# Kernel optimization log

Hardware: AMD Instinct MI355X
Metric: run time of the kernel (lower is better)

## Reference

```python
import jax, jax.numpy as jnp
import numpy as np
import math

LATENT = 64
COMP = 20
EM_ITERS = 5
GAMMA1 = 1.0  # 1/sqrt(gamma), gamma=1
LOG_NORM_C = -0.5 * math.log(2.0 * math.pi)


def setup_inputs() -> dict:
    key = jax.random.key(0)
    k1, k2, k3 = jax.random.split(key, 3)
    z = jax.random.normal(k1, (64, 8192, LATENT), dtype=jnp.float32)
    # small causal adjacency so (I - A) and the inverses are well conditioned
    A = jax.random.normal(k2, (LATENT, LATENT), dtype=jnp.float32) * 0.05
    init_idx = jax.random.randint(k3, (64, COMP), 0, 8192)
    return {"z": z, "A": A, "init_idx": init_idx}


def _em_step(X, pi, mean, trace, IA):
    # X: [B,N,L], pi/trace: [B,K], mean: [B,K,L], IA = I - A: [L,L]
    B, N, L = X.shape
    # gaussian_log_prob(X, mean) with logvar=0, summed over L, expanded as
    # -0.5*||x-m||^2 + L*c, computed without materializing a [B,N,K,L] tensor
    sq_x = jnp.sum(X * X, axis=-1)                      # [B,N]
    sq_m = jnp.sum(mean * mean, axis=-1)                # [B,K]
    cross = jnp.einsum('bnl,bkl->bnk', X, mean)         # [B,N,K]
    term_x = -0.5 * (sq_x[:, :, None] - 2.0 * cross + sq_m[:, None, :]) + L * LOG_NORM_C
    # gaussian_log_prob(causal(mean), 0, logvar=log(trace) broadcast over L)
    cm = jnp.einsum('bkl,lm->bkm', mean, IA)            # causal(mean)
    lt = jnp.log(trace)                                  # [B,K]
    term_c = -0.5 * (L * lt + jnp.sum(cm * cm, axis=-1) / trace) + L * LOG_NORM_C
    ll = term_x + jnp.log(pi)[:, None, :] + term_c[:, None, :]   # [B,N,K]
    post = jax.nn.softmax(ll, axis=-1)
    Nk = jnp.sum(post, axis=1)                           # [B,K]
    Nk = jnp.where(Nk == 0.0, jnp.asarray(1e-22, Nk.dtype), Nk)
    new_trace = GAMMA1 * jnp.ones_like(Nk)
    # std_causal = causal(I*trace) = trace*(I-A); trace is gamma1 for every
    # (b,k), so the [B,K,L,L] inverse collapses to one shared [L,L] inverse.
    I = jnp.eye(L, dtype=X.dtype)
    M = jnp.linalg.inv(I + (GAMMA1 ** 2) * (IA @ IA.T))
    new_pi = Nk / jnp.sum(Nk, axis=-1, keepdims=True)    # fix_pi=False
    new_mean = jnp.einsum('bnk,bnl->bkl', post, X) / Nk[:, :, None]
    new_mean = jnp.einsum('bkl,lm->bkm', new_mean, M)
    return new_pi, new_mean, new_trace


def reference(z, A, init_idx):
    # EM-based Gaussian-mixture prior (get_unsupervised_prior) of GMVAE
    B, N, L = z.shape
    I = jnp.eye(L, dtype=z.dtype)
    IA = I - A  # linear CausalEncoder: causal(x) = x @ (I - A)
    pi = jnp.full((B, COMP), 1.0 / COMP, dtype=z.dtype)
    trace = jnp.ones((B, COMP), dtype=z.dtype)
    # initial inverse: inv(I + (1/trace) * sig_cas @ sig_cas.T), trace == 1
    M0 = jnp.linalg.inv(I + IA @ IA.T)
    mean = jnp.take_along_axis(z, init_idx[:, :, None], axis=1)  # [B,K,L]
    mean = jnp.einsum('bkl,lm->bkm', mean, M0)
    for _ in range(EM_ITERS):
        pi, mean, trace = _em_step(z, pi, mean, trace, IA)
    return pi, mean, trace
```

## Files before the change

### kernel.cpp

```cpp
#include <hip/hip_runtime.h>
#include <math.h>

#define BB 64
#define NN 8192
#define LL 64
#define KK 20
#define TILE 128
#define NT 8
#define CHUNKS 8
#define ZSB 72
#define ZTS 140
#define PTTS 136
#define AS 132
#define TS 68

typedef float f32x4 __attribute__((ext_vector_type(4)));
typedef short s16x8 __attribute__((ext_vector_type(8)));
typedef short s16x4 __attribute__((ext_vector_type(4)));
typedef unsigned short u16x4 __attribute__((ext_vector_type(4)));
typedef unsigned short u16x2 __attribute__((ext_vector_type(2)));

#define MFMA_BF16 __builtin_amdgcn_mfma_f32_16x16x32_bf16

__device__ __forceinline__ unsigned short f2bf(float f) {
    unsigned int u = __float_as_uint(f);
    u += 0x7fffu + ((u >> 16) & 1u);
    return (unsigned short)(u >> 16);
}
__device__ __forceinline__ float bf2f(unsigned short h) {
    return __uint_as_float(((unsigned int)h) << 16);
}


__global__ __launch_bounds__(256) void k_setup(const float* __restrict__ A,
                                               float* __restrict__ IA,
                                               float* __restrict__ M) {
    __shared__ __align__(16) float iaT[64][TS];
    __shared__ __align__(16) float aug[64][AS];
    __shared__ __align__(16) float prowbuf[2][AS];
    int t = threadIdx.x;
    for (int i = t; i < 4096; i += 256) {
        int r = i >> 6, c = i & 63;
        float v = (r == c ? 1.0f : 0.0f) - A[i];
        IA[i] = v;
        iaT[c][r] = v;
    }
    __syncthreads();
    {
        int r0 = (t >> 4) << 2;
        int c0 = (t & 15) << 2;
        float s[4][4];
        #pragma unroll
        for (int a = 0; a < 4; ++a)
            #pragma unroll
            for (int bq = 0; bq < 4; ++bq) s[a][bq] = 0.f;
        for (int l = 0; l < 64; ++l) {
            float4 u = *(const float4*)&iaT[l][r0];
            float4 v = *(const float4*)&iaT[l][c0];
            float uu[4] = {u.x, u.y, u.z, u.w};
            float vv[4] = {v.x, v.y, v.z, v.w};
            #pragma unroll
            for (int a = 0; a < 4; ++a)
                #pragma unroll
                for (int bq = 0; bq < 4; ++bq) s[a][bq] += uu[a] * vv[bq];
        }
        #pragma unroll
        for (int a = 0; a < 4; ++a) {
            int r = r0 + a;
            float4 w;
            w.x = s[a][0] + (r == c0 + 0 ? 1.f : 0.f);
            w.y = s[a][1] + (r == c0 + 1 ? 1.f : 0.f);
            w.z = s[a][2] + (r == c0 + 2 ? 1.f : 0.f);
            w.w = s[a][3] + (r == c0 + 3 ? 1.f : 0.f);
            *(float4*)&aug[r][c0] = w;
            float4 id;
            id.x = (r == c0 + 0 ? 1.f : 0.f);
            id.y = (r == c0 + 1 ? 1.f : 0.f);
            id.z = (r == c0 + 2 ? 1.f : 0.f);
            id.w = (r == c0 + 3 ? 1.f : 0.f);
            *(float4*)&aug[r][64 + c0] = id;
        }
    }
    __syncthreads();
    int r = t >> 2;
    int cbase = (t & 3) * 32;
    if (r == 0) {
        float pivinv = 1.0f / aug[0][0];
        #pragma unroll
        for (int i = 0; i < 8; ++i) {
            float4 v = *(const float4*)&aug[0][cbase + 4 * i];
            v.x *= pivinv; v.y *= pivinv; v.z *= pivinv; v.w *= pivinv;
            *(float4*)&prowbuf[0][cbase + 4 * i] = v;
        }
    }
    __syncthreads();
    for (int k = 0; k < 64; ++k) {
        const float* prow = prowbuf[k & 1];
        float* prown = prowbuf[(k + 1) & 1];
        if (r == k) {
            #pragma unroll
            for (int i = 0; i < 8; ++i)
                *(float4*)&aug[r][cbase + 4 * i] = *(const float4*)&prow[cbase + 4 * i];
        } else {
            float f = aug[r][k];
            float4 v[8];
            #pragma unroll
            for (int i = 0; i < 8; ++i) {
                float4 p = *(const float4*)&prow[cbase + 4 * i];
                float4 a = *(const float4*)&aug[r][cbase + 4 * i];
                a.x -= f * p.x; a.y -= f * p.y; a.z -= f * p.z; a.w -= f * p.w;
                *(float4*)&aug[r][cbase + 4 * i] = a;
                v[i] = a;
            }
            if (r == k + 1) {
                float pivinv = 1.0f / aug[k + 1][k + 1];
                #pragma unroll
                for (int i = 0; i < 8; ++i) {
                    float4 w = v[i];
                    w.x *= pivinv; w.y *= pivinv; w.z *= pivinv; w.w *= pivinv;
                    *(float4*)&prown[cbase + 4 * i] = w;
                }
            }
        }
        __syncthreads();
    }
    for (int i = t; i < 4096; i += 256) {
        int rr = i >> 6, c = i & 63;
        M[i] = aug[rr][64 + c];
    }
}

__global__ __launch_bounds__(64) void k_init(const float* __restrict__ z,
                                             const int* __restrict__ idxs,
                                             const float* __restrict__ M,
                                             const float* __restrict__ IA,
                                             float* __restrict__ out_mean,
                                             float* __restrict__ bias,
                                             float* __restrict__ nk,
                                             float* __restrict__ macc,
                                             int* __restrict__ cnt) {
    int k = blockIdx.x, b = blockIdx.y;
    int l = threadIdx.x;
    int bk = b * KK + k;
    __shared__ float srow[64];
    __shared__ float smean[64];
    int idx = idxs[bk];
    srow[l] = z[((size_t)b * NN + idx) * LL + l];
    __syncthreads();
    float nm = 0.f;
    #pragma unroll 8
    for (int m = 0; m < 64; ++m) nm += srow[m] * M[m * 64 + l];
    out_mean[(size_t)bk * LL + l] = nm;
    smean[l] = nm;
    __syncthreads();
    float cm = 0.f;
    #pragma unroll 8
    for (int m = 0; m < 64; ++m) cm += smean[m] * IA[m * 64 + l];
    float sqm = nm * nm;
    float sqc = cm * cm;
    for (int off = 32; off > 0; off >>= 1) {
        sqm += __shfl_down(sqm, off);
        sqc += __shfl_down(sqc, off);
    }
    if (l == 0) {
        bias[bk] = logf(1.0f / KK) - 0.5f * (sqm + sqc);
        nk[bk] = 0.f;
        if (k == 0) cnt[b] = 0;
    }
    macc[(size_t)bk * LL + l] = 0.f;
}

__global__ __launch_bounds__(256, 2) void k_empass(const float* __restrict__ z,
                                                   float* __restrict__ mean,
                                                   float* __restrict__ bias,
                                                   float* __restrict__ nk,
                                                   float* __restrict__ macc,
                                                   int* __restrict__ cnt,
                                                   const float* __restrict__ M,
                                                   const float* __restrict__ IA,
                                                   float* __restrict__ out_pi,
                                                   float* __restrict__ out_trace) {
    __shared__ __align__(16) unsigned short zhl[2][TILE][ZSB];
    __shared__ __align__(16) unsigned short mhl[2][32][ZSB];
    __shared__ __align__(16) unsigned short zT[64][ZTS];
    __shared__ __align__(16) unsigned short ptT[32][PTTS];
    __shared__ __align__(16) float bias_s[32];
    __shared__ float nkred[4][KK];
    __shared__ int isLast;
    int t = threadIdx.x;
    int lane = t & 63;
    int q = t >> 6;
    int ln = lane & 15;
    int lg4 = lane >> 4;
    int s = t & 15;
    int b = blockIdx.y;
    size_t zbase = ((size_t)b * NN + (size_t)blockIdx.x * (TILE * NT)) * LL;

    for (int i = t; i < KK * LL; i += 256) {
        float f = mean[(size_t)b * KK * LL + i];
        int k = i >> 6, c = i & 63;
        unsigned short h = f2bf(f);
        mhl[0][k][c] = h;
        mhl[1][k][c] = f2bf(f - bf2f(h));
    }
    for (int i = 20 * ZSB + t; i < 32 * ZSB; i += 256) {
        (&mhl[0][0][0])[i] = 0;
        (&mhl[1][0][0])[i] = 0;
    }
    {
        unsigned int* pz = (unsigned int*)&ptT[20][0];
        for (int i = t; i < 6 * PTTS; i += 256) pz[i] = 0;
    }
    if (t < 32) bias_s[t] = (t < KK) ? bias[b * KK + t] : -1e30f;
    __syncthreads();
    float4 b0 = *(const float4*)&bias_s[lg4 * 4];
    float4 b1 = *(const float4*)&bias_s[16 + lg4 * 4];

    const float4* zg = (const float4*)(z + zbase);
    f32x4 bacc0 = {0.f, 0.f, 0.f, 0.f};
    f32x4 bacc1 = {0.f, 0.f, 0.f, 0.f};
    float nkp0[4] = {0.f, 0.f, 0.f, 0.f};
    float nkp1[4] = {0.f, 0.f, 0.f, 0.f};

    for (int tt = 0; tt < NT; ++tt) {
        if (tt > 0) __syncthreads();
        #pragma unroll
        for (int u = 0; u < 4; ++u) {
            int r0 = u * 32 + ((t >> 4) << 1);
            float4 v0 = zg[tt * 2048 + r0 * 16 + s];
            float4 v1 = zg[tt * 2048 + (r0 + 1) * 16 + s];
            unsigned short h0 = f2bf(v0.x), h1 = f2bf(v0.y), h2 = f2bf(v0.z), h3 = f2bf(v0.w);
            unsigned short g0 = f2bf(v1.x), g1 = f2bf(v1.y), g2 = f2bf(v1.z), g3 = f2bf(v1.w);
            *(u16x4*)&zhl[0][r0][4 * s]     = (u16x4){h0, h1, h2, h3};
            *(u16x4*)&zhl[0][r0 + 1][4 * s] = (u16x4){g0, g1, g2, g3};
            *(u16x4*)&zhl[1][r0][4 * s]     = (u16x4){f2bf(v0.x - bf2f(h0)), f2bf(v0.y - bf2f(h1)),
                                                      f2bf(v0.z - bf2f(h2)), f2bf(v0.w - bf2f(h3))};
            *(u16x4*)&zhl[1][r0 + 1][4 * s] = (u16x4){f2bf(v1.x - bf2f(g0)), f2bf(v1.y - bf2f(g1)),
                                                      f2bf(v1.z - bf2f(g2)), f2bf(v1.w - bf2f(g3))};
            *(u16x2*)&zT[4 * s + 0][r0] = (u16x2){h0, g0};
            *(u16x2*)&zT[4 * s + 1][r0] = (u16x2){h1, g1};
            *(u16x2*)&zT[4 * s + 2][r0] = (u16x2){h2, g2};
            *(u16x2*)&zT[4 * s + 3][r0] = (u16x2){h3, g3};
        }
        __syncthreads();

        f32x4 acc0[2], acc1[2];
        #pragma unroll
        for (int rt = 0; rt < 2; ++rt) {
            acc0[rt] = (f32x4){b0.x, b0.y, b0.z, b0.w};
            acc1[rt] = (f32x4){b1.x, b1.y, b1.z, b1.w};
        }
        #pragma unroll
        for (int ks = 0; ks < 2; ++ks) {
            int kc = ks * 32 + lg4 * 8;
            s16x8 mh0 = *(const s16x8*)&mhl[0][ln][kc];
            s16x8 ml0 = *(const s16x8*)&mhl[1][ln][kc];
            s16x8 mh1 = *(const s16x8*)&mhl[0][16 + ln][kc];
            s16x8 ml1 = *(const s16x8*)&mhl[1][16 + ln][kc];
            #pragma unroll
            for (int rt = 0; rt < 2; ++rt) {
                int zrow = q * 32 + rt * 16 + ln;
                s16x8 zh = *(const s16x8*)&zhl[0][zrow][kc];
                s16x8 zl = *(const s16x8*)&zhl[1][zrow][kc];
                acc0[rt] = MFMA_BF16(mh0, zh, acc0[rt], 0, 0, 0);
                acc0[rt] = MFMA_BF16(ml0, zh, acc0[rt], 0, 0, 0);
                acc0[rt] = MFMA_BF16(mh0, zl, acc0[rt], 0, 0, 0);
                acc1[rt] = MFMA_BF16(mh1, zh, acc1[rt], 0, 0, 0);
                acc1[rt] = MFMA_BF16(ml1, zh, acc1[rt], 0, 0, 0);
                acc1[rt] = MFMA_BF16(mh1, zl, acc1[rt], 0, 0, 0);
            }
        }
        #pragma unroll
        for (int rt = 0; rt < 2; ++rt) {
            int zrow = q * 32 + rt * 16 + ln;
            float m = fmaxf(fmaxf(fmaxf(acc0[rt][0], acc0[rt][1]), fmaxf(acc0[rt][2], acc0[rt][3])),
                            fmaxf(fmaxf(acc1[rt][0], acc1[rt][1]), fmaxf(acc1[rt][2], acc1[rt][3])));
            m = fmaxf(m, __shfl_xor(m, 16));
            m = fmaxf(m, __shfl_xor(m, 32));
            float e0[4], e1[4];
            float sm = 0.f;
            #pragma unroll
            for (int j = 0; j < 4; ++j) {
                e0[j] = __expf(acc0[rt][j] - m); sm += e0[j];
                e1[j] = __expf(acc1[rt][j] - m); sm += e1[j];
            }
            sm += __shfl_xor(sm, 16);
            sm += __shfl_xor(sm, 32);
            float inv = 1.0f / sm;
            #pragma unroll
            for (int j = 0; j < 4; ++j) {
                float p = e0[j] * inv;
                nkp0[j] += p;
                ptT[lg4 * 4 + j][zrow] = f2bf(p);
            }
            if (lg4 == 0) {
                #pragma unroll
                for (int j = 0; j < 4; ++j) {
                    float p = e1[j] * inv;
                    nkp1[j] += p;
                    ptT[16 + j][zrow] = f2bf(p);
                }
            }
        }
        __syncthreads();

        #pragma unroll
        for (int ch = 0; ch < 4; ++ch) {
            int rr = ch * 32 + lg4 * 8;
            s16x4 zb0 = *(const s16x4*)&zT[q * 16 + ln][rr];
            s16x4 zb1 = *(const s16x4*)&zT[q * 16 + ln][rr + 4];
            s16x8 bfr = (s16x8){zb0[0], zb0[1], zb0[2], zb0[3], zb1[0], zb1[1], zb1[2], zb1[3]};
            s16x8 af0 = *(const s16x8*)&ptT[ln][rr];
            s16x8 af1 = *(const s16x8*)&ptT[16 + ln][rr];
            bacc0 = MFMA_BF16(af0, bfr, bacc0, 0, 0, 0);
            bacc1 = MFMA_BF16(af1, bfr, bacc1, 0, 0, 0);
        }
    }

    #pragma unroll
    for (int j = 0; j < 4; ++j) {
        nkp0[j] += __shfl_xor(nkp0[j], 1);
        nkp0[j] += __shfl_xor(nkp0[j], 2);
        nkp0[j] += __shfl_xor(nkp0[j], 4);
        nkp0[j] += __shfl_xor(nkp0[j], 8);
    }
    if (ln == 0) {
        #pragma unroll
        for (int j = 0; j < 4; ++j) nkred[q][lg4 * 4 + j] = nkp0[j];
    }
    if (lg4 == 0) {
        #pragma unroll
        for (int j = 0; j < 4; ++j) {
            nkp1[j] += __shfl_xor(nkp1[j], 1);
            nkp1[j] += __shfl_xor(nkp1[j], 2);
            nkp1[j] += __shfl_xor(nkp1[j], 4);
            nkp1[j] += __shfl_xor(nkp1[j], 8);
        }
        if (ln == 0) {
            #pragma unroll
            for (int j = 0; j < 4; ++j) nkred[q][16 + j] = nkp1[j];
        }
    }

    int col = q * 16 + ln;
    #pragma unroll
    for (int reg = 0; reg < 4; ++reg) {
        int comp = lg4 * 4 + reg;
        atomicAdd(&macc[((size_t)b * KK + comp) * LL + col], bacc0[reg]);
    }
    if (lg4 == 0) {
        #pragma unroll
        for (int reg = 0; reg < 4; ++reg)
            atomicAdd(&macc[((size_t)b * KK + 16 + reg) * LL + col], bacc1[reg]);
    }
    __syncthreads();
    if (t < KK) {
        float sum = nkred[0][t] + nkred[1][t] + nkred[2][t] + nkred[3][t];
        atomicAdd(&nk[b * KK + t], sum);
    }
    __syncthreads();
    if (t == 0) {
        __threadfence();
        int old = atomicAdd(&cnt[b], 1);
        isLast = (old == CHUNKS - 1) ? 1 : 0;
    }
    __syncthreads();
    if (!isLast) return;

    float* fs = (float*)&zhl[0][0][0];
    float* sraw = fs + q * 160;
    float* smean = sraw + 64;
    int l = lane;
    #pragma unroll
    for (int kc5 = 0; kc5 < 5; ++kc5) {
        int comp = kc5 * 4 + q;
        int bk = b * KK + comp;
        size_t mb = (size_t)bk * LL;
        float nkv = 0.f;
        if (l == 0) nkv = atomicExch(&nk[bk], 0.f);
        nkv = __shfl(nkv, 0);
        float nkc = fmaxf(nkv, 1e-22f);
        float raw = atomicExch(&macc[mb + l], 0.f) / nkc;
        sraw[l] = raw;
        float nm = 0.f;
        #pragma unroll 8
        for (int m = 0; m < 64; ++m) nm += sraw[m] * M[m * 64 + l];
        mean[mb + l] = nm;
        smean[l] = nm;
        float cm = 0.f;
        #pragma unroll 8
        for (int m = 0; m < 64; ++m) cm += smean[m] * IA[m * 64 + l];
        float sqm = nm * nm;
        float sqc = cm * cm;
        #pragma unroll
        for (int off = 32; off > 0; off >>= 1) {
            sqm += __shfl_down(sqm, off);
            sqc += __shfl_down(sqc, off);
        }
        if (l == 0) {
            float pi = nkc * (1.0f / NN);
            bias[bk] = logf(pi) - 0.5f * (sqm + sqc);
            out_pi[bk] = pi;
            out_trace[bk] = 1.0f;
        }
    }
    if (t == 0) cnt[b] = 0;
}

extern "C" void kernel_launch(void* const* d_in, const int* in_sizes, int n_in,
                              void* d_out, int out_size, void* d_ws, size_t ws_size,
                              hipStream_t stream) {
    const float* z = (const float*)d_in[0];
    const float* A = (const float*)d_in[1];
    const int* idxs = (const int*)d_in[2];

    float* out_pi = (float*)d_out;
    float* out_mean = out_pi + BB * KK;
    float* out_trace = out_mean + (size_t)BB * KK * LL;

    float* ws = (float*)d_ws;
    float* IA = ws;
    float* M = ws + 4096;
    float* bias = ws + 8192;
    float* nk = ws + 9472;
    float* macc = ws + 10752;
    int* cnt = (int*)(ws + 92672);

    k_setup<<<1, 256, 0, stream>>>(A, IA, M);
    k_init<<<dim3(KK, BB), 64, 0, stream>>>(z, idxs, M, IA, out_mean, bias, nk, macc, cnt);
    for (int it = 0; it < 5; ++it) {
        k_empass<<<dim3(CHUNKS, BB), 256, 0, stream>>>(z, out_mean, bias, nk, macc,
                                                       cnt, M, IA, out_pi, out_trace);
    }
}
```

Measured before the change: 377.3 us.

## Prefetch z tiles into registers, hoist mean fragments, use Newton-Schulz inverse

The main EM kernel now loads the next z tile into registers while it computes on the current one, then writes that tile to shared memory after the MFMA stage, with one fewer barrier per tile. The mean bf16 fragments are hoisted into registers outside the tile loop. The softmax write path is made branch-free, and the zero-fill of the padded rows of the posterior tile is removed. The setup kernel replaces serial Gauss-Jordan elimination with 8 Newton-Schulz iterations made of 64x64 matmuls. This shortens the setup critical path but adds an approximation risk if convergence is incomplete, and the mainloop keeps more values live in registers.

```diff
diff --git a/kernel.cpp b/kernel.cpp
--- a/kernel.cpp
+++ b/kernel.cpp
@@ -11,8 +11,7 @@
 #define ZSB 72
 #define ZTS 140
 #define PTTS 136
-#define AS 132
-#define TS 68
+#define NSS 68
 
 typedef float f32x4 __attribute__((ext_vector_type(4)));
 typedef short s16x8 __attribute__((ext_vector_type(8)));
@@ -35,34 +34,39 @@
 __global__ __launch_bounds__(256) void k_setup(const float* __restrict__ A,
                                                float* __restrict__ IA,
                                                float* __restrict__ M) {
-    __shared__ __align__(16) float iaT[64][TS];
-    __shared__ __align__(16) float aug[64][AS];
-    __shared__ __align__(16) float prowbuf[2][AS];
+    __shared__ __align__(16) float sS[64][NSS];
+    __shared__ __align__(16) float sXa[64][NSS];
+    __shared__ __align__(16) float sXb[64][NSS];
+    __shared__ __align__(16) float sT[64][NSS];
+    __shared__ float rowsum[64];
+    __shared__ float alpha_s;
     int t = threadIdx.x;
+    int r0 = (t >> 4) << 2;
+    int c0 = (t & 15) << 2;
+
     for (int i = t; i < 4096; i += 256) {
         int r = i >> 6, c = i & 63;
         float v = (r == c ? 1.0f : 0.0f) - A[i];
         IA[i] = v;
-        iaT[c][r] = v;
+        sT[c][r] = v;
     }
     __syncthreads();
     {
-        int r0 = (t >> 4) << 2;
-        int c0 = (t & 15) << 2;
         float s[4][4];
         #pragma unroll
         for (int a = 0; a < 4; ++a)
             #pragma unroll
-            for (int bq = 0; bq < 4; ++bq) s[a][bq] = 0.f;
+            for (int b = 0; b < 4; ++b) s[a][b] = 0.f;
+        #pragma unroll 4
         for (int l = 0; l < 64; ++l) {
-            float4 u = *(const float4*)&iaT[l][r0];
-            float4 v = *(const float4*)&iaT[l][c0];
+            float4 u = *(const float4*)&sT[l][r0];
+            float4 v = *(const float4*)&sT[l][c0];
             float uu[4] = {u.x, u.y, u.z, u.w};
             float vv[4] = {v.x, v.y, v.z, v.w};
             #pragma unroll
             for (int a = 0; a < 4; ++a)
                 #pragma unroll
-                for (int bq = 0; bq < 4; ++bq) s[a][bq] += uu[a] * vv[bq];
+                for (int b = 0; b < 4; ++b) s[a][b] += uu[a] * vv[b];
         }
         #pragma unroll
         for (int a = 0; a < 4; ++a) {
@@ -72,62 +76,91 @@
             w.y = s[a][1] + (r == c0 + 1 ? 1.f : 0.f);
             w.z = s[a][2] + (r == c0 + 2 ? 1.f : 0.f);
             w.w = s[a][3] + (r == c0 + 3 ? 1.f : 0.f);
-            *(float4*)&aug[r][c0] = w;
-            float4 id;
-            id.x = (r == c0 + 0 ? 1.f : 0.f);
-            id.y = (r == c0 + 1 ? 1.f : 0.f);
-            id.z = (r == c0 + 2 ? 1.f : 0.f);
-            id.w = (r == c0 + 3 ? 1.f : 0.f);
-            *(float4*)&aug[r][64 + c0] = id;
-        }
-    }
-    __syncthreads();
-    int r = t >> 2;
-    int cbase = (t & 3) * 32;
-    if (r == 0) {
-        float pivinv = 1.0f / aug[0][0];
-        #pragma unroll
-        for (int i = 0; i < 8; ++i) {
-            float4 v = *(const float4*)&aug[0][cbase + 4 * i];
-            v.x *= pivinv; v.y *= pivinv; v.z *= pivinv; v.w *= pivinv;
-            *(float4*)&prowbuf[0][cbase + 4 * i] = v;
-        }
-    }
-    __syncthreads();
-    for (int k = 0; k < 64; ++k) {
-        const float* prow = prowbuf[k & 1];
-        float* prown = prowbuf[(k + 1) & 1];
-        if (r == k) {
-            #pragma unroll
-            for (int i = 0; i < 8; ++i)
-                *(float4*)&aug[r][cbase + 4 * i] = *(const float4*)&prow[cbase + 4 * i];
-        } else {
-            float f = aug[r][k];
-            float4 v[8];
-            #pragma unroll
-            for (int i = 0; i < 8; ++i) {
-                float4 p = *(const float4*)&prow[cbase + 4 * i];
-                float4 a = *(const float4*)&aug[r][cbase + 4 * i];
-                a.x -= f * p.x; a.y -= f * p.y; a.z -= f * p.z; a.w -= f * p.w;
-                *(float4*)&aug[r][cbase + 4 * i] = a;
-                v[i] = a;
-            }
-            if (r == k + 1) {
-                float pivinv = 1.0f / aug[k + 1][k + 1];
+            *(float4*)&sS[r][c0] = w;
+        }
+    }
+    __syncthreads();
+    if (t < 64) {
+        float sm = 0.f;
+        #pragma unroll 4
+        for (int c = 0; c < 64; c += 4) {
+            float4 v = *(const float4*)&sS[t][c];
+            sm += fabsf(v.x) + fabsf(v.y) + fabsf(v.z) + fabsf(v.w);
+        }
+        rowsum[t] = sm;
+    }
+    __syncthreads();
+    if (t == 0) {
+        float mx = rowsum[0];
+        for (int i = 1; i < 64; ++i) mx = fmaxf(mx, rowsum[i]);
+        alpha_s = 2.0f / (1.0f + mx);
+    }
+    __syncthreads();
+    float alpha = alpha_s;
+    for (int i = t; i < 4096; i += 256) {
+        int r = i >> 6, c = i & 63;
+        sXa[r][c] = (r == c) ? alpha : 0.f;
+    }
+    __syncthreads();
+
+    float* X  = &sXa[0][0];
+    float* Xn = &sXb[0][0];
+    for (int it = 0; it < 8; ++it) {
+        {
+            float s[4][4];
+            #pragma unroll
+            for (int a = 0; a < 4; ++a)
                 #pragma unroll
-                for (int i = 0; i < 8; ++i) {
-                    float4 w = v[i];
-                    w.x *= pivinv; w.y *= pivinv; w.z *= pivinv; w.w *= pivinv;
-                    *(float4*)&prown[cbase + 4 * i] = w;
-                }
-            }
+                for (int b = 0; b < 4; ++b) s[a][b] = 0.f;
+            #pragma unroll 4
+            for (int k = 0; k < 64; ++k) {
+                float4 u = *(const float4*)&sS[k][r0];
+                float4 v = *(const float4*)&X[k * NSS + c0];
+                float uu[4] = {u.x, u.y, u.z, u.w};
+                float vv[4] = {v.x, v.y, v.z, v.w};
+                #pragma unroll
+                for (int a = 0; a < 4; ++a)
+                    #pragma unroll
+                    for (int b = 0; b < 4; ++b) s[a][b] += uu[a] * vv[b];
+            }
+            #pragma unroll
+            for (int a = 0; a < 4; ++a)
+                *(float4*)&sT[r0 + a][c0] = (float4){s[a][0], s[a][1], s[a][2], s[a][3]};
         }
         __syncthreads();
-    }
-    for (int i = t; i < 4096; i += 256) {
-        int rr = i >> 6, c = i & 63;
-        M[i] = aug[rr][64 + c];
-    }
+        {
+            float s[4][4];
+            #pragma unroll
+            for (int a = 0; a < 4; ++a)
+                #pragma unroll
+                for (int b = 0; b < 4; ++b) s[a][b] = 0.f;
+            #pragma unroll 4
+            for (int k = 0; k < 64; ++k) {
+                float4 u = *(const float4*)&X[k * NSS + r0];
+                float4 v = *(const float4*)&sT[k][c0];
+                float uu[4] = {u.x, u.y, u.z, u.w};
+                float vv[4] = {v.x, v.y, v.z, v.w};
+                #pragma unroll
+                for (int a = 0; a < 4; ++a)
+                    #pragma unroll
+                    for (int b = 0; b < 4; ++b) s[a][b] += uu[a] * vv[b];
+            }
+            #pragma unroll
+            for (int a = 0; a < 4; ++a) {
+                float4 xo = *(const float4*)&X[(r0 + a) * NSS + c0];
+                float4 w;
+                w.x = 2.f * xo.x - s[a][0];
+                w.y = 2.f * xo.y - s[a][1];
+                w.z = 2.f * xo.z - s[a][2];
+                w.w = 2.f * xo.w - s[a][3];
+                *(float4*)&Xn[(r0 + a) * NSS + c0] = w;
+            }
+        }
+        __syncthreads();
+        float* tmp = X; X = Xn; Xn = tmp;
+    }
+    for (int i = t; i < 4096; i += 256)
+        M[i] = X[(i >> 6) * NSS + (i & 63)];
 }
 
 __global__ __launch_bounds__(64) void k_init(const float* __restrict__ z,
@@ -192,9 +225,9 @@
     int q = t >> 6;
     int ln = lane & 15;
     int lg4 = lane >> 4;
-    int s = t & 15;
     int b = blockIdx.y;
     size_t zbase = ((size_t)b * NN + (size_t)blockIdx.x * (TILE * NT)) * LL;
+    int rbase = 32 * q + 8 * lg4;
 
     for (int i = t; i < KK * LL; i += 256) {
         float f = mean[(size_t)b * KK * LL + i];
@@ -207,42 +240,77 @@
         (&mhl[0][0][0])[i] = 0;
         (&mhl[1][0][0])[i] = 0;
     }
-    {
-        unsigned int* pz = (unsigned int*)&ptT[20][0];
-        for (int i = t; i < 6 * PTTS; i += 256) pz[i] = 0;
-    }
     if (t < 32) bias_s[t] = (t < KK) ? bias[b * KK + t] : -1e30f;
     __syncthreads();
     float4 b0 = *(const float4*)&bias_s[lg4 * 4];
     float4 b1 = *(const float4*)&bias_s[16 + lg4 * 4];
+    s16x8 mf[8];
+    #pragma unroll
+    for (int ks = 0; ks < 2; ++ks) {
+        int kc = ks * 32 + lg4 * 8;
+        mf[ks * 4 + 0] = *(const s16x8*)&mhl[0][ln][kc];
+        mf[ks * 4 + 1] = *(const s16x8*)&mhl[1][ln][kc];
+        mf[ks * 4 + 2] = *(const s16x8*)&mhl[0][16 + ln][kc];
+        mf[ks * 4 + 3] = *(const s16x8*)&mhl[1][16 + ln][kc];
+    }
 
     const float4* zg = (const float4*)(z + zbase);
+    float4 pf[8];
+
+#define LOADT(tt)                                                              \
+    {                                                                          \
+        _Pragma("unroll")                                                      \
+        for (int u = 0; u < 4; ++u) {                                          \
+            int r0_ = rbase + 2 * u;                                           \
+            pf[2 * u]     = zg[(size_t)(tt) * 2048 + r0_ * 16 + ln];           \
+            pf[2 * u + 1] = zg[(size_t)(tt) * 2048 + (r0_ + 1) * 16 + ln];     \
+        }                                                                      \
+    }
+#define WRITE_ZHL                                                              \
+    {                                                                          \
+        _Pragma("unroll")                                                      \
+        for (int u = 0; u < 4; ++u) {                                          \
+            int r0_ = rbase + 2 * u;                                           \
+            float4 v0 = pf[2 * u], v1 = pf[2 * u + 1];                         \
+            unsigned short h0 = f2bf(v0.x), h1 = f2bf(v0.y),                   \
+                           h2 = f2bf(v0.z), h3 = f2bf(v0.w);                   \
+            unsigned short g0 = f2bf(v1.x), g1 = f2bf(v1.y),                   \
+                           g2 = f2bf(v1.z), g3 = f2bf(v1.w);                   \
+            *(u16x4*)&zhl[0][r0_][4 * ln]     = (u16x4){h0, h1, h2, h3};       \
+            *(u16x4*)&zhl[0][r0_ + 1][4 * ln] = (u16x4){g0, g1, g2, g3};       \
+            *(u16x4*)&zhl[1][r0_][4 * ln] =                                    \
+                (u16x4){f2bf(v0.x - bf2f(h0)), f2bf(v0.y - bf2f(h1)),          \
+                        f2bf(v0.z - bf2f(h2)), f2bf(v0.w - bf2f(h3))};         \
+            *(u16x4*)&zhl[1][r0_ + 1][4 * ln] =                                \
+                (u16x4){f2bf(v1.x - bf2f(g0)), f2bf(v1.y - bf2f(g1)),          \
+                        f2bf(v1.z - bf2f(g2)), f2bf(v1.w - bf2f(g3))};         \
+        }                                                                      \
+    }
+#define WRITE_ZT                                                               \
+    {                                                                          \
+        _Pragma("unroll")                                                      \
+        for (int u = 0; u < 4; ++u) {                                          \
+            int r0_ = rbase + 2 * u;                                           \
+            float4 v0 = pf[2 * u], v1 = pf[2 * u + 1];                         \
+            *(u16x2*)&zT[4 * ln + 0][r0_] = (u16x2){f2bf(v0.x), f2bf(v1.x)};   \
+            *(u16x2*)&zT[4 * ln + 1][r0_] = (u16x2){f2bf(v0.y), f2bf(v1.y)};   \
+            *(u16x2*)&zT[4 * ln + 2][r0_] = (u16x2){f2bf(v0.z), f2bf(v1.z)};   \
+            *(u16x2*)&zT[4 * ln + 3][r0_] = (u16x2){f2bf(v0.w), f2bf(v1.w)};   \
+        }                                                                      \
+    }
+
+    LOADT(0);
+    WRITE_ZHL;
+    WRITE_ZT;
+    __syncthreads();
+
     f32x4 bacc0 = {0.f, 0.f, 0.f, 0.f};
     f32x4 bacc1 = {0.f, 0.f, 0.f, 0.f};
     float nkp0[4] = {0.f, 0.f, 0.f, 0.f};
     float nkp1[4] = {0.f, 0.f, 0.f, 0.f};
 
     for (int tt = 0; tt < NT; ++tt) {
-        if (tt > 0) __syncthreads();
-        #pragma unroll
-        for (int u = 0; u < 4; ++u) {
-            int r0 = u * 32 + ((t >> 4) << 1);
-            float4 v0 = zg[tt * 2048 + r0 * 16 + s];
-            float4 v1 = zg[tt * 2048 + (r0 + 1) * 16 + s];
-            unsigned short h0 = f2bf(v0.x), h1 = f2bf(v0.y), h2 = f2bf(v0.z), h3 = f2bf(v0.w);
-            unsigned short g0 = f2bf(v1.x), g1 = f2bf(v1.y), g2 = f2bf(v1.z), g3 = f2bf(v1.w);
-            *(u16x4*)&zhl[0][r0][4 * s]     = (u16x4){h0, h1, h2, h3};
-            *(u16x4*)&zhl[0][r0 + 1][4 * s] = (u16x4){g0, g1, g2, g3};
-            *(u16x4*)&zhl[1][r0][4 * s]     = (u16x4){f2bf(v0.x - bf2f(h0)), f2bf(v0.y - bf2f(h1)),
-                                                      f2bf(v0.z - bf2f(h2)), f2bf(v0.w - bf2f(h3))};
-            *(u16x4*)&zhl[1][r0 + 1][4 * s] = (u16x4){f2bf(v1.x - bf2f(g0)), f2bf(v1.y - bf2f(g1)),
-                                                      f2bf(v1.z - bf2f(g2)), f2bf(v1.w - bf2f(g3))};
-            *(u16x2*)&zT[4 * s + 0][r0] = (u16x2){h0, g0};
-            *(u16x2*)&zT[4 * s + 1][r0] = (u16x2){h1, g1};
-            *(u16x2*)&zT[4 * s + 2][r0] = (u16x2){h2, g2};
-            *(u16x2*)&zT[4 * s + 3][r0] = (u16x2){h3, g3};
-        }
-        __syncthreads();
+        if (tt + 1 < NT) LOADT(tt + 1);
 
         f32x4 acc0[2], acc1[2];
         #pragma unroll
@@ -253,21 +321,17 @@
         #pragma unroll
         for (int ks = 0; ks < 2; ++ks) {
             int kc = ks * 32 + lg4 * 8;
-            s16x8 mh0 = *(const s16x8*)&mhl[0][ln][kc];
-            s16x8 ml0 = *(const s16x8*)&mhl[1][ln][kc];
-            s16x8 mh1 = *(const s16x8*)&mhl[0][16 + ln][kc];
-            s16x8 ml1 = *(const s16x8*)&mhl[1][16 + ln][kc];
             #pragma unroll
             for (int rt = 0; rt < 2; ++rt) {
                 int zrow = q * 32 + rt * 16 + ln;
                 s16x8 zh = *(const s16x8*)&zhl[0][zrow][kc];
                 s16x8 zl = *(const s16x8*)&zhl[1][zrow][kc];
-                acc0[rt] = MFMA_BF16(mh0, zh, acc0[rt], 0, 0, 0);
-                acc0[rt] = MFMA_BF16(ml0, zh, acc0[rt], 0, 0, 0);
-                acc0[rt] = MFMA_BF16(mh0, zl, acc0[rt], 0, 0, 0);
-                acc1[rt] = MFMA_BF16(mh1, zh, acc1[rt], 0, 0, 0);
-                acc1[rt] = MFMA_BF16(ml1, zh, acc1[rt], 0, 0, 0);
-                acc1[rt] = MFMA_BF16(mh1, zl, acc1[rt], 0, 0, 0);
+                acc0[rt] = MFMA_BF16(mf[ks * 4 + 0], zh, acc0[rt], 0, 0, 0);
+                acc0[rt] = MFMA_BF16(mf[ks * 4 + 1], zh, acc0[rt], 0, 0, 0);
+                acc0[rt] = MFMA_BF16(mf[ks * 4 + 0], zl, acc0[rt], 0, 0, 0);
+                acc1[rt] = MFMA_BF16(mf[ks * 4 + 2], zh, acc1[rt], 0, 0, 0);
+                acc1[rt] = MFMA_BF16(mf[ks * 4 + 3], zh, acc1[rt], 0, 0, 0);
+                acc1[rt] = MFMA_BF16(mf[ks * 4 + 2], zl, acc1[rt], 0, 0, 0);
             }
         }
         #pragma unroll
@@ -289,17 +353,12 @@
             float inv = 1.0f / sm;
             #pragma unroll
             for (int j = 0; j < 4; ++j) {
-                float p = e0[j] * inv;
-                nkp0[j] += p;
-                ptT[lg4 * 4 + j][zrow] = f2bf(p);
-            }
-            if (lg4 == 0) {
-                #pragma unroll
-                for (int j = 0; j < 4; ++j) {
-                    float p = e1[j] * inv;
-                    nkp1[j] += p;
-                    ptT[16 + j][zrow] = f2bf(p);
-                }
+                float p0 = e0[j] * inv;
+                float p1 = e1[j] * inv;
+                nkp0[j] += p0;
+                nkp1[j] += p1;
+                ptT[lg4 * 4 + j][zrow] = f2bf(p0);
+                ptT[16 + lg4 * 4 + j][zrow] = f2bf(p1);
             }
         }
         __syncthreads();
@@ -315,6 +374,9 @@
             bacc0 = MFMA_BF16(af0, bfr, bacc0, 0, 0, 0);
             bacc1 = MFMA_BF16(af1, bfr, bacc1, 0, 0, 0);
         }
+        if (tt + 1 < NT) WRITE_ZHL;
+        __syncthreads();
+        if (tt + 1 < NT) WRITE_ZT;
     }
 
     #pragma unroll
@@ -323,20 +385,15 @@
         nkp0[j] += __shfl_xor(nkp0[j], 2);
         nkp0[j] += __shfl_xor(nkp0[j], 4);
         nkp0[j] += __shfl_xor(nkp0[j], 8);
+        nkp1[j] += __shfl_xor(nkp1[j], 1);
+        nkp1[j] += __shfl_xor(nkp1[j], 2);
+        nkp1[j] += __shfl_xor(nkp1[j], 4);
+        nkp1[j] += __shfl_xor(nkp1[j], 8);
     }
     if (ln == 0) {
         #pragma unroll
         for (int j = 0; j < 4; ++j) nkred[q][lg4 * 4 + j] = nkp0[j];
-    }
-    if (lg4 == 0) {
-        #pragma unroll
-        for (int j = 0; j < 4; ++j) {
-            nkp1[j] += __shfl_xor(nkp1[j], 1);
-            nkp1[j] += __shfl_xor(nkp1[j], 2);
-            nkp1[j] += __shfl_xor(nkp1[j], 4);
-            nkp1[j] += __shfl_xor(nkp1[j], 8);
-        }
-        if (ln == 0) {
+        if (lg4 == 0) {
             #pragma unroll
             for (int j = 0; j < 4; ++j) nkred[q][16 + j] = nkp1[j];
         }
@@ -405,6 +462,9 @@
         }
     }
     if (t == 0) cnt[b] = 0;
+#undef LOADT
+#undef WRITE_ZHL
+#undef WRITE_ZT
 }
 
 extern "C" void kernel_launch(void* const* d_in, const int* in_sizes, int n_in,
```

Measured after the change: 335.0 us. 1.13x faster.
